# Performance work log

Hardware: AMD Instinct MI355X
Metric: run time of the kernel (lower is better)

Reference implementation:

```python
import jax, jax.numpy as jnp
import numpy as np

B, C_IN, C_OUT, K, H, W = 8, 512, 512, 3, 32, 32
EPS = 1e-8


def _fir_filter():
    f1 = jnp.array([1.0, 3.0, 3.0, 1.0], dtype=jnp.float32)
    f = jnp.outer(f1, f1)
    f = f / f.sum()
    return f * 4.0  # gain = 2**2, filter.ndim/2 == 1


def setup_inputs() -> dict:
    key = jax.random.key(0)
    k1, k2, k3 = jax.random.split(key, 3)
    x = jax.random.normal(k1, (B, C_IN, H, W), dtype=jnp.float32)
    styles = jax.random.normal(k2, (B, C_IN), dtype=jnp.float32)
    w = jax.random.normal(k3, (C_OUT, C_IN, K, K), dtype=jnp.float32)  # lr_multiplier=1
    return {"x": x, "styles": styles, "w": w}


def reference(x, styles, w):
    batch = x.shape[0]
    gain = 1.0 / np.sqrt(C_OUT * C_IN * K * K)
    # modulate: [B, O, I, kh, kw]
    wm = (w[None] * gain) * (styles[:, None, :, None, None] + 1.0)
    # demodulate
    dcoefs = jax.lax.rsqrt(jnp.sum(wm * wm, axis=(2, 3, 4)) + EPS)  # [B, O]
    wm = wm * dcoefs[:, :, None, None, None]
    # fused modconv: batch folded into channels/groups
    x1 = x.reshape(1, batch * C_IN, H, W)
    # torch conv_transpose2d(stride=2, padding=0, groups=B) == dilated conv with
    # spatially flipped kernel, lhs_dilation=2, padding=K-1 on each side.
    w_eq = jnp.flip(wm, axis=(-2, -1)).reshape(batch * C_OUT, C_IN, K, K)
    y = jax.lax.conv_general_dilated(
        x1, w_eq,
        window_strides=(1, 1),
        padding=[(K - 1, K - 1), (K - 1, K - 1)],
        lhs_dilation=(2, 2),
        feature_group_count=batch,
        dimension_numbers=("NCHW", "OIHW", "NCHW"),
    )  # [1, B*O, 2H+1, 2W+1]
    # Upfirdn2d: up=1, down=1, pad=[1,1,1,1], depthwise 4x4 FIR (cross-correlation;
    # filter is symmetric so no flip needed)
    C = batch * C_OUT
    f = jnp.broadcast_to(_fir_filter()[None, None], (C, 1, 4, 4))
    y = jax.lax.conv_general_dilated(
        y, f,
        window_strides=(1, 1),
        padding=[(1, 1), (1, 1)],
        feature_group_count=C,
        dimension_numbers=("NCHW", "OIHW", "NCHW"),
    )  # [1, B*O, 2H, 2W]
    return y.reshape(batch, C_OUT, 2 * H, 2 * W)
```

## Files before the change

kernel.cpp:

```cpp
#include <hip/hip_runtime.h>
#include <stdint.h>


#define DI __device__ __forceinline__

typedef __bf16 bf16x8 __attribute__((ext_vector_type(8)));
typedef float f32x4 __attribute__((ext_vector_type(4)));

DI float bf2f(ushort u) { union { uint32_t i; float f; } v; v.i = ((uint32_t)u) << 16; return v.f; }
DI ushort f2bf(float f) {
  union { float f; uint32_t i; } v; v.f = f;
  uint32_t x = v.i;
  return (ushort)((x + 0x7FFFu + ((x >> 16) & 1u)) >> 16);
}

#define GAIN (1.0f / 1536.0f)

__global__ __launch_bounds__(256) void k_q(const float* __restrict__ w,
                                           float* __restrict__ q) {
  const int gid = blockIdx.x * 256 + threadIdx.x;
  const float* p = w + gid * 9;
  float s = 0.f;
#pragma unroll
  for (int t = 0; t < 9; t++) s += p[t] * p[t];
  q[gid] = s;
}

__global__ __launch_bounds__(256) void k_dcoef(const float* __restrict__ q,
                                               const float* __restrict__ styles,
                                               float* __restrict__ dcoef) {
  const int bo = blockIdx.x * 4 + (threadIdx.x >> 6);
  const int b = bo >> 9, o = bo & 511;
  const int lane = threadIdx.x & 63;
  float sum = 0.f;
#pragma unroll
  for (int j = 0; j < 8; j++) {
    const int i = lane + j * 64;
    float s = styles[b * 512 + i] + 1.0f;
    sum += s * s * q[o * 512 + i];
  }
#pragma unroll
  for (int off = 32; off > 0; off >>= 1) sum += __shfl_down(sum, off, 64);
  if (lane == 0) dcoef[bo] = rsqrtf(sum * (GAIN * GAIN) + 1e-8f);
}

__global__ __launch_bounds__(256) void k_wmprep(const float* __restrict__ w,
                                                const float* __restrict__ styles,
                                                const float* __restrict__ dcoef,
                                                ushort* __restrict__ Wm) {
  const int gid = blockIdx.x * 256 + threadIdx.x;
  const int o = gid >> 9, i = gid & 511;
  float wf[9];
#pragma unroll
  for (int t = 0; t < 9; t++) wf[t] = w[gid * 9 + t];
  for (int b = 0; b < 8; b++) {
    float s = styles[b * 512 + i];
    float d = dcoef[b * 512 + o];
    float scale = GAIN * (s + 1.0f) * d;
#pragma unroll
    for (int t = 0; t < 9; t++) Wm[(((b * 9 + t) * 512 + o) << 9) + i] = f2bf(wf[t] * scale);
  }
}

__global__ __launch_bounds__(256) void k_xt(const float* __restrict__ x,
                                            ushort* __restrict__ xt) {
  __shared__ float t[32][33];
  const int b = blockIdx.z, hw0 = blockIdx.x * 32, i0 = blockIdx.y * 32;
  const int tx = threadIdx.x & 31, ty = threadIdx.x >> 5;
  const float* xb = x + b * (512 * 1024);
#pragma unroll
  for (int r = 0; r < 4; r++) t[ty + r * 8][tx] = xb[(i0 + ty + r * 8) * 1024 + hw0 + tx];
  __syncthreads();
  ushort* xtb = xt + b * (1024 * 512);
#pragma unroll
  for (int r = 0; r < 4; r++) xtb[(hw0 + ty + r * 8) * 512 + i0 + tx] = f2bf(t[tx][ty + r * 8]);
}

__global__ __launch_bounds__(256) void k_gemm(const ushort* __restrict__ A,
                                              const ushort* __restrict__ Bt,
                                              ushort* __restrict__ C) {
  __shared__ __attribute__((aligned(16))) char smem[32768];
  const int id = blockIdx.x;
  const int batch = id & 7;
  const int rem = id >> 3;
  const int tap = rem >> 5;
  const int t = rem & 31;
  const int mt = t >> 3, nt = t & 7;
  const int g = batch * 9 + tap;
  const ushort* Ag = A + g * (512 * 512);
  const ushort* Bg = Bt + batch * (1024 * 512);
  ushort* Cg = C + g * (512 * 1024);
  const int tid = threadIdx.x;
  const int lane = tid & 63, wv = tid >> 6;
  const int m0 = mt * 128, n0 = nt * 128;
  const int wm2 = wv >> 1, wn2 = wv & 1;
  const int lq = lane >> 4, l15 = lane & 15;
  const int l4 = lane & 3, ld4 = lane >> 2;
  const int r0 = (0 * 4 + wv) * 16 + ld4;
  const int r1 = (1 * 4 + wv) * 16 + ld4;

  const ushort* pA0 = Ag + (m0 + r0) * 512 + l4 * 8;
  const ushort* pA1 = Ag + (m0 + r1) * 512 + l4 * 8;
  const ushort* pB0 = Bg + (n0 + r0) * 512 + l4 * 8;
  const ushort* pB1 = Bg + (n0 + r1) * 512 + l4 * 8;
  char* dA0 = smem + (0 * 4 + wv) * 1024;
  char* dA1 = smem + (1 * 4 + wv) * 1024;
  char* dB0 = smem + 8192 + (0 * 4 + wv) * 1024;
  char* dB1 = smem + 8192 + (1 * 4 + wv) * 1024;

#define ISSUE(buf, kc)                                                                        \
  do {                                                                                        \
    __builtin_amdgcn_global_load_lds((const __attribute__((address_space(1))) void*)(pA0 + (kc)), \
                                     (__attribute__((address_space(3))) void*)(dA0 + (buf)*16384), 16, 0, 0); \
    __builtin_amdgcn_global_load_lds((const __attribute__((address_space(1))) void*)(pA1 + (kc)), \
                                     (__attribute__((address_space(3))) void*)(dA1 + (buf)*16384), 16, 0, 0); \
    __builtin_amdgcn_global_load_lds((const __attribute__((address_space(1))) void*)(pB0 + (kc)), \
                                     (__attribute__((address_space(3))) void*)(dB0 + (buf)*16384), 16, 0, 0); \
    __builtin_amdgcn_global_load_lds((const __attribute__((address_space(1))) void*)(pB1 + (kc)), \
                                     (__attribute__((address_space(3))) void*)(dB1 + (buf)*16384), 16, 0, 0); \
  } while (0)

  const char* abase = smem + (wm2 * 64 + l15) * 64 + lq * 16;
  const char* bbase = smem + 8192 + (wn2 * 64 + l15) * 64 + lq * 16;

  f32x4 zero = {0.f, 0.f, 0.f, 0.f};
  f32x4 acc[4][4];
#pragma unroll
  for (int mi = 0; mi < 4; mi++)
#pragma unroll
    for (int ni = 0; ni < 4; ni++) acc[mi][ni] = zero;

  ISSUE(0, 0);
  for (int it = 0; it < 16; ++it) {
    __syncthreads();
    const int cur = it & 1;
    if (it < 15) ISSUE(cur ^ 1, (it + 1) * 32);
    const int bo = cur * 16384;
    bf16x8 af[4], bfr[4];
#pragma unroll
    for (int mi = 0; mi < 4; mi++) af[mi] = *(const bf16x8*)(abase + bo + mi * 1024);
#pragma unroll
    for (int ni = 0; ni < 4; ni++) bfr[ni] = *(const bf16x8*)(bbase + bo + ni * 1024);
#pragma unroll
    for (int mi = 0; mi < 4; mi++)
#pragma unroll
      for (int ni = 0; ni < 4; ni++)
        acc[mi][ni] = __builtin_amdgcn_mfma_f32_16x16x32_bf16(af[mi], bfr[ni], acc[mi][ni], 0, 0, 0);
  }
#undef ISSUE
#pragma unroll
  for (int mi = 0; mi < 4; mi++) {
#pragma unroll
    for (int ni = 0; ni < 4; ni++) {
      const int row = m0 + wm2 * 64 + mi * 16 + lq * 4;
      const int col = n0 + wn2 * 64 + ni * 16 + l15;
      f32x4 v = acc[mi][ni];
#pragma unroll
      for (int r = 0; r < 4; r++) Cg[(row + r) * 1024 + col] = f2bf(v[r]);
    }
  }
}

__global__ __launch_bounds__(256) void k_fir(const ushort* __restrict__ C,
                                             float* __restrict__ out) {
  const int bo = blockIdx.x;
  const int b = bo >> 9, o = bo & 511;
  __shared__ __attribute__((aligned(16))) ushort Ct[9 * 1024];
  __shared__ float V[3 * 64 * 32];
  __shared__ int rb[64][6];
  __shared__ float rc[64][6];
  __shared__ int cb[64][6];
  __shared__ float cc[64][6];
  const ushort* Cb = C + ((size_t)(b * 9) * 512 + o) * 1024;
  for (int c = threadIdx.x; c < 1152; c += 256) {
    const int tap = c >> 7, off = (c & 127) * 8;
    *(uint4*)&Ct[tap * 1024 + off] = *(const uint4*)&Cb[(size_t)tap * 524288 + off];
  }
  const float F[4] = {1.f, 3.f, 3.f, 1.f};
  if (threadIdx.x < 64) {
    const int u = threadIdx.x;
    int n = 0;
    for (int kh = 0; kh < 3; kh++)
      for (int s = 0; s < 4; s++) {
        int num = u + s - 1 - kh;
        if (num & 1) continue;
        int h = num >> 1;
        bool val = (h >= 0 && h < 32);
        rb[u][n] = val ? kh * 3072 + h * 32 : 0;
        rc[u][n] = val ? F[s] : 0.f;
        n++;
      }
  } else if (threadIdx.x < 128) {
    const int v = threadIdx.x - 64;
    int n = 0;
    for (int kw = 0; kw < 3; kw++)
      for (int t = 0; t < 4; t++) {
        int num = v + t - 1 - kw;
        if (num & 1) continue;
        int w = num >> 1;
        bool val = (w >= 0 && w < 32);
        cb[v][n] = val ? kw * 2048 + w : 0;
        cc[v][n] = val ? F[t] : 0.f;
        n++;
      }
  }
  __syncthreads();
#pragma unroll
  for (int j = 0; j < 6; j++) {
    const int gidx = threadIdx.x + j * 256;
    const int kw = gidx >> 9;
    const int rem = gidx & 511;
    const int u = rem >> 3;
    const int w0 = (rem & 7) * 4;
    float a0 = 0.f, a1 = 0.f, a2 = 0.f, a3 = 0.f;
#pragma unroll
    for (int n = 0; n < 6; n++) {
      const float cf = rc[u][n];
      const ushort* p = &Ct[rb[u][n] + kw * 1024 + w0];
      a0 += cf * bf2f(p[0]);
      a1 += cf * bf2f(p[1]);
      a2 += cf * bf2f(p[2]);
      a3 += cf * bf2f(p[3]);
    }
    float4* vp = (float4*)&V[kw * 2048 + u * 32 + w0];
    *vp = make_float4(a0, a1, a2, a3);
  }
  __syncthreads();
  const size_t ob = (size_t)bo * 4096;
#pragma unroll
  for (int j = 0; j < 16; j++) {
    const int px = threadIdx.x + j * 256;
    const int u = px >> 6, v = px & 63;
    float s = 0.f;
#pragma unroll
    for (int n = 0; n < 6; n++) s += cc[v][n] * V[cb[v][n] + u * 32];
    out[ob + px] = s * 0.0625f;
  }
}

extern "C" void kernel_launch(void* const* d_in, const int* in_sizes, int n_in,
                              void* d_out, int out_size, void* d_ws, size_t ws_size,
                              hipStream_t stream) {
  (void)in_sizes; (void)n_in; (void)out_size; (void)ws_size;
  const float* x = (const float*)d_in[0];
  const float* styles = (const float*)d_in[1];
  const float* w = (const float*)d_in[2];
  float* out = (float*)d_out;
  char* ws = (char*)d_ws;
  float* dcoef = (float*)ws;
  ushort* Wm = (ushort*)(ws + 16384);
  ushort* XT = (ushort*)(ws + 16384 + 37748736);
  ushort* C = (ushort*)(ws + 16384 + 37748736 + 8388608);
  float* q = (float*)(ws + 16384 + 37748736 + 8388608 + 75497472);

  k_q<<<1024, 256, 0, stream>>>(w, q);
  k_dcoef<<<1024, 256, 0, stream>>>(q, styles, dcoef);
  k_wmprep<<<1024, 256, 0, stream>>>(w, styles, dcoef, Wm);
  k_xt<<<dim3(32, 16, 8), 256, 0, stream>>>(x, XT);
  k_gemm<<<2304, 256, 0, stream>>>(Wm, XT, C);
  k_fir<<<4096, 256, 0, stream>>>(C, out);
}
```

Measured before the change: 179.1 us.

## Fuse weight prep kernels, vectorize transpose and GEMM stores, inline FIR tables

Merges the three weight-preparation kernels (sum of squares, demod coefficients, modulated bf16 weights) into one per-output-channel kernel that reduces in registers and shared memory, which removes two launches and the round trips through global memory. The x transpose now uses float4 loads and ushort4 stores over wider tiles. The GEMM epilogue stages the bf16 results in shared memory so it can write coalesced 16-byte rows. The FIR kernel drops its shared-memory index and coefficient tables, computes the taps inline, and writes float4 outputs. These changes add more index arithmetic and an extra barrier in the GEMM.

After: 167.0 us. 1.07x faster.

```diff
diff --git a/kernel.cpp b/kernel.cpp
--- a/kernel.cpp
+++ b/kernel.cpp
@@ -16,64 +16,91 @@
 
 #define GAIN (1.0f / 1536.0f)
 
-__global__ __launch_bounds__(256) void k_q(const float* __restrict__ w,
-                                           float* __restrict__ q) {
-  const int gid = blockIdx.x * 256 + threadIdx.x;
-  const float* p = w + gid * 9;
-  float s = 0.f;
-#pragma unroll
-  for (int t = 0; t < 9; t++) s += p[t] * p[t];
-  q[gid] = s;
-}
-
-__global__ __launch_bounds__(256) void k_dcoef(const float* __restrict__ q,
+__global__ __launch_bounds__(256) void k_wprep(const float* __restrict__ w,
                                                const float* __restrict__ styles,
-                                               float* __restrict__ dcoef) {
-  const int bo = blockIdx.x * 4 + (threadIdx.x >> 6);
-  const int b = bo >> 9, o = bo & 511;
-  const int lane = threadIdx.x & 63;
-  float sum = 0.f;
-#pragma unroll
-  for (int j = 0; j < 8; j++) {
-    const int i = lane + j * 64;
-    float s = styles[b * 512 + i] + 1.0f;
-    sum += s * s * q[o * 512 + i];
-  }
-#pragma unroll
-  for (int off = 32; off > 0; off >>= 1) sum += __shfl_down(sum, off, 64);
-  if (lane == 0) dcoef[bo] = rsqrtf(sum * (GAIN * GAIN) + 1e-8f);
-}
-
-__global__ __launch_bounds__(256) void k_wmprep(const float* __restrict__ w,
-                                                const float* __restrict__ styles,
-                                                const float* __restrict__ dcoef,
-                                                ushort* __restrict__ Wm) {
-  const int gid = blockIdx.x * 256 + threadIdx.x;
-  const int o = gid >> 9, i = gid & 511;
-  float wf[9];
-#pragma unroll
-  for (int t = 0; t < 9; t++) wf[t] = w[gid * 9 + t];
+                                               ushort* __restrict__ Wm) {
+  const int o = blockIdx.x;
+  const int t = threadIdx.x;
+  __shared__ float ss[4096];
+  __shared__ float dc[8];
+  __shared__ float wred[4][8];
+#pragma unroll
+  for (int j = 0; j < 4; j++) {
+    const int idx = (t + j * 256) * 4;
+    *(float4*)&ss[idx] = *(const float4*)&styles[idx];
+  }
+  float wreg[18];
+  const float* wp = w + o * 4608 + t * 18;
+#pragma unroll
+  for (int k = 0; k < 9; k++) {
+    float2 v2 = *(const float2*)(wp + 2 * k);
+    wreg[2 * k] = v2.x;
+    wreg[2 * k + 1] = v2.y;
+  }
+  float q0 = 0.f, q1 = 0.f;
+#pragma unroll
+  for (int k = 0; k < 9; k++) {
+    q0 += wreg[k] * wreg[k];
+    q1 += wreg[9 + k] * wreg[9 + k];
+  }
+  __syncthreads();
+  float pb[8];
+#pragma unroll
   for (int b = 0; b < 8; b++) {
-    float s = styles[b * 512 + i];
-    float d = dcoef[b * 512 + o];
-    float scale = GAIN * (s + 1.0f) * d;
-#pragma unroll
-    for (int t = 0; t < 9; t++) Wm[(((b * 9 + t) * 512 + o) << 9) + i] = f2bf(wf[t] * scale);
+    float s0 = ss[b * 512 + 2 * t] + 1.0f;
+    float s1 = ss[b * 512 + 2 * t + 1] + 1.0f;
+    pb[b] = s0 * s0 * q0 + s1 * s1 * q1;
+  }
+#pragma unroll
+  for (int b = 0; b < 8; b++)
+#pragma unroll
+    for (int off = 32; off > 0; off >>= 1) pb[b] += __shfl_down(pb[b], off, 64);
+  const int wid = t >> 6, lane = t & 63;
+  if (lane == 0) {
+#pragma unroll
+    for (int b = 0; b < 8; b++) wred[wid][b] = pb[b];
+  }
+  __syncthreads();
+  if (t < 8)
+    dc[t] = rsqrtf((wred[0][t] + wred[1][t] + wred[2][t] + wred[3][t]) * (GAIN * GAIN) + 1e-8f);
+  __syncthreads();
+#pragma unroll
+  for (int b = 0; b < 8; b++) {
+    const float d = dc[b];
+    const float s0 = GAIN * (ss[b * 512 + 2 * t] + 1.0f) * d;
+    const float s1 = GAIN * (ss[b * 512 + 2 * t + 1] + 1.0f) * d;
+    ushort* base = Wm + ((size_t)(b * 9) * 512 + o) * 512 + 2 * t;
+#pragma unroll
+    for (int tap = 0; tap < 9; tap++) {
+      ushort2 val = make_ushort2(f2bf(wreg[tap] * s0), f2bf(wreg[9 + tap] * s1));
+      *(ushort2*)(base + (size_t)tap * 262144) = val;
+    }
   }
 }
 
 __global__ __launch_bounds__(256) void k_xt(const float* __restrict__ x,
                                             ushort* __restrict__ xt) {
-  __shared__ float t[32][33];
-  const int b = blockIdx.z, hw0 = blockIdx.x * 32, i0 = blockIdx.y * 32;
-  const int tx = threadIdx.x & 31, ty = threadIdx.x >> 5;
+  __shared__ float tl[32][257];
+  const int b = blockIdx.z, i0 = blockIdx.y * 32, hw0 = blockIdx.x * 256;
+  const int t = threadIdx.x;
   const float* xb = x + b * (512 * 1024);
 #pragma unroll
-  for (int r = 0; r < 4; r++) t[ty + r * 8][tx] = xb[(i0 + ty + r * 8) * 1024 + hw0 + tx];
+  for (int p = 0; p < 8; p++) {
+    const int r = p * 4 + (t >> 6);
+    const int c4 = (t & 63) * 4;
+    float4 v = *(const float4*)&xb[(i0 + r) * 1024 + hw0 + c4];
+    tl[r][c4] = v.x; tl[r][c4 + 1] = v.y; tl[r][c4 + 2] = v.z; tl[r][c4 + 3] = v.w;
+  }
   __syncthreads();
   ushort* xtb = xt + b * (1024 * 512);
 #pragma unroll
-  for (int r = 0; r < 4; r++) xtb[(hw0 + ty + r * 8) * 512 + i0 + tx] = f2bf(t[tx][ty + r * 8]);
+  for (int p = 0; p < 8; p++) {
+    const int hw = p * 32 + (t >> 3);
+    const int i4 = (t & 7) * 4;
+    ushort4 v = make_ushort4(f2bf(tl[i4][hw]), f2bf(tl[i4 + 1][hw]),
+                             f2bf(tl[i4 + 2][hw]), f2bf(tl[i4 + 3][hw]));
+    *(ushort4*)&xtb[(hw0 + hw) * 512 + i0 + i4] = v;
+  }
 }
 
 __global__ __launch_bounds__(256) void k_gemm(const ushort* __restrict__ A,
@@ -148,16 +175,25 @@
         acc[mi][ni] = __builtin_amdgcn_mfma_f32_16x16x32_bf16(af[mi], bfr[ni], acc[mi][ni], 0, 0, 0);
   }
 #undef ISSUE
+  __syncthreads();
+  ushort* cs = (ushort*)smem;
 #pragma unroll
   for (int mi = 0; mi < 4; mi++) {
 #pragma unroll
     for (int ni = 0; ni < 4; ni++) {
-      const int row = m0 + wm2 * 64 + mi * 16 + lq * 4;
-      const int col = n0 + wn2 * 64 + ni * 16 + l15;
+      const int row = wm2 * 64 + mi * 16 + lq * 4;
+      const int col = wn2 * 64 + ni * 16 + l15;
       f32x4 v = acc[mi][ni];
 #pragma unroll
-      for (int r = 0; r < 4; r++) Cg[(row + r) * 1024 + col] = f2bf(v[r]);
-    }
+      for (int r = 0; r < 4; r++) cs[(row + r) * 128 + col] = f2bf(v[r]);
+    }
+  }
+  __syncthreads();
+#pragma unroll
+  for (int p = 0; p < 8; p++) {
+    const int r2 = p * 16 + (tid >> 4);
+    const int c8 = (tid & 15) * 8;
+    *(uint4*)(Cg + (m0 + r2) * 1024 + n0 + c8) = *(const uint4*)(cs + r2 * 128 + c8);
   }
 }
 
@@ -167,42 +203,10 @@
   const int b = bo >> 9, o = bo & 511;
   __shared__ __attribute__((aligned(16))) ushort Ct[9 * 1024];
   __shared__ float V[3 * 64 * 32];
-  __shared__ int rb[64][6];
-  __shared__ float rc[64][6];
-  __shared__ int cb[64][6];
-  __shared__ float cc[64][6];
   const ushort* Cb = C + ((size_t)(b * 9) * 512 + o) * 1024;
   for (int c = threadIdx.x; c < 1152; c += 256) {
     const int tap = c >> 7, off = (c & 127) * 8;
     *(uint4*)&Ct[tap * 1024 + off] = *(const uint4*)&Cb[(size_t)tap * 524288 + off];
-  }
-  const float F[4] = {1.f, 3.f, 3.f, 1.f};
-  if (threadIdx.x < 64) {
-    const int u = threadIdx.x;
-    int n = 0;
-    for (int kh = 0; kh < 3; kh++)
-      for (int s = 0; s < 4; s++) {
-        int num = u + s - 1 - kh;
-        if (num & 1) continue;
-        int h = num >> 1;
-        bool val = (h >= 0 && h < 32);
-        rb[u][n] = val ? kh * 3072 + h * 32 : 0;
-        rc[u][n] = val ? F[s] : 0.f;
-        n++;
-      }
-  } else if (threadIdx.x < 128) {
-    const int v = threadIdx.x - 64;
-    int n = 0;
-    for (int kw = 0; kw < 3; kw++)
-      for (int t = 0; t < 4; t++) {
-        int num = v + t - 1 - kw;
-        if (num & 1) continue;
-        int w = num >> 1;
-        bool val = (w >= 0 && w < 32);
-        cb[v][n] = val ? kw * 2048 + w : 0;
-        cc[v][n] = val ? F[t] : 0.f;
-        n++;
-      }
   }
   __syncthreads();
 #pragma unroll
@@ -214,27 +218,48 @@
     const int w0 = (rem & 7) * 4;
     float a0 = 0.f, a1 = 0.f, a2 = 0.f, a3 = 0.f;
 #pragma unroll
-    for (int n = 0; n < 6; n++) {
-      const float cf = rc[u][n];
-      const ushort* p = &Ct[rb[u][n] + kw * 1024 + w0];
-      a0 += cf * bf2f(p[0]);
-      a1 += cf * bf2f(p[1]);
-      a2 += cf * bf2f(p[2]);
-      a3 += cf * bf2f(p[3]);
-    }
-    float4* vp = (float4*)&V[kw * 2048 + u * 32 + w0];
-    *vp = make_float4(a0, a1, a2, a3);
+    for (int kh = 0; kh < 3; kh++) {
+      const int s0 = (kh + 1 + u) & 1;
+#pragma unroll
+      for (int d = 0; d < 2; d++) {
+        const int h = (u + s0 + 2 * d - 1 - kh) >> 1;
+        const bool ok = (h >= 0) & (h < 32);
+        const float cf = ok ? ((s0 == d) ? 1.f : 3.f) : 0.f;
+        const int hh = ok ? h : 0;
+        const uint2 cv = *(const uint2*)&Ct[kh * 3072 + kw * 1024 + hh * 32 + w0];
+        a0 += cf * bf2f((ushort)(cv.x & 0xffff));
+        a1 += cf * bf2f((ushort)(cv.x >> 16));
+        a2 += cf * bf2f((ushort)(cv.y & 0xffff));
+        a3 += cf * bf2f((ushort)(cv.y >> 16));
+      }
+    }
+    *(float4*)&V[kw * 2048 + u * 32 + w0] = make_float4(a0, a1, a2, a3);
   }
   __syncthreads();
   const size_t ob = (size_t)bo * 4096;
 #pragma unroll
-  for (int j = 0; j < 16; j++) {
-    const int px = threadIdx.x + j * 256;
-    const int u = px >> 6, v = px & 63;
-    float s = 0.f;
-#pragma unroll
-    for (int n = 0; n < 6; n++) s += cc[v][n] * V[cb[v][n] + u * 32];
-    out[ob + px] = s * 0.0625f;
+  for (int p = 0; p < 4; p++) {
+    const int u = p * 16 + (threadIdx.x >> 4);
+    const int v0 = (threadIdx.x & 15) * 4;
+    float r[4] = {0.f, 0.f, 0.f, 0.f};
+#pragma unroll
+    for (int q = 0; q < 4; q++) {
+      const int v = v0 + q;
+#pragma unroll
+      for (int kw = 0; kw < 3; kw++) {
+        const int t0 = (kw + 1 + v) & 1;
+#pragma unroll
+        for (int d = 0; d < 2; d++) {
+          const int w = (v + t0 + 2 * d - 1 - kw) >> 1;
+          const bool ok = (w >= 0) & (w < 32);
+          const float cf = ok ? ((t0 == d) ? 1.f : 3.f) : 0.f;
+          const int ww = ok ? w : 0;
+          r[q] += cf * V[kw * 2048 + u * 32 + ww];
+        }
+      }
+      r[q] *= 0.0625f;
+    }
+    *(float4*)&out[ob + u * 64 + v0] = make_float4(r[0], r[1], r[2], r[3]);
   }
 }
 
@@ -247,16 +272,12 @@
   const float* w = (const float*)d_in[2];
   float* out = (float*)d_out;
   char* ws = (char*)d_ws;
-  float* dcoef = (float*)ws;
-  ushort* Wm = (ushort*)(ws + 16384);
-  ushort* XT = (ushort*)(ws + 16384 + 37748736);
-  ushort* C = (ushort*)(ws + 16384 + 37748736 + 8388608);
-  float* q = (float*)(ws + 16384 + 37748736 + 8388608 + 75497472);
-
-  k_q<<<1024, 256, 0, stream>>>(w, q);
-  k_dcoef<<<1024, 256, 0, stream>>>(q, styles, dcoef);
-  k_wmprep<<<1024, 256, 0, stream>>>(w, styles, dcoef, Wm);
-  k_xt<<<dim3(32, 16, 8), 256, 0, stream>>>(x, XT);
+  ushort* Wm = (ushort*)ws;
+  ushort* XT = (ushort*)(ws + 37748736);
+  ushort* C = (ushort*)(ws + 37748736 + 8388608);
+
+  k_wprep<<<512, 256, 0, stream>>>(w, styles, Wm);
+  k_xt<<<dim3(4, 16, 8), 256, 0, stream>>>(x, XT);
   k_gemm<<<2304, 256, 0, stream>>>(Wm, XT, C);
   k_fir<<<4096, 256, 0, stream>>>(C, out);
 }
```
